# Kernel optimization log

Measured on AMD Instinct MI355X. Metric: run time of the kernel, lower is better.

Reference implementation:

```python
import jax, jax.numpy as jnp
import numpy as np

H, W = 64, 64

def _fft_mask(h, w):
    # matches torch: W -> W//2+1 for rfft; linspace(-1,1,H) x linspace(0,1,W//2+1)
    wr = w // 2 + 1
    ys = np.linspace(-1.0, 1.0, h)
    xs = np.linspace(0.0, 1.0, wr)
    Y, X = np.meshgrid(ys, xs, indexing='ij')
    return (np.abs(X) < 0.1) | (np.abs(Y) < 0.1) | (X ** 2 + Y ** 2 <= 0.4 ** 2)

_MASK = _fft_mask(H, W)
_IY, _IX = np.nonzero(_MASK)            # static gather indices, K = mask.sum()
_K = int(_MASK.sum())


def setup_inputs() -> dict:
    key = jax.random.key(0)
    k1, k2, k3 = jax.random.split(key, 3)
    S, P, C = 16, 256, 3
    enc_dim = 1024
    mask_dim = 6 * _K                    # real+imag, C=3 channels -> 2*3*K
    x = jax.random.normal(k1, (S, P, C, H, W), dtype=jnp.float32)
    bc_mask = jnp.zeros((H, W), dtype=bool)
    proj_w = jax.random.normal(k2, (enc_dim, mask_dim), dtype=jnp.float32) / np.sqrt(mask_dim)
    proj_b = jax.random.normal(k3, (enc_dim,), dtype=jnp.float32) * 0.01
    return {"x": x, "bc_mask": bc_mask, "proj_w": proj_w, "proj_b": proj_b}


def reference(x, bc_mask, proj_w, proj_b):
    S, P, C = x.shape[0], x.shape[1], x.shape[2]
    fft_x = jnp.fft.rfft2(x)                       # (S,P,C,H,W//2+1) complex
    fft_x = jnp.fft.fftshift(fft_x, axes=-2)       # shift along H
    # boolean-mask gather (row-major over (H, W//2+1) per (s,p,c)), then flatten C*K
    filt = fft_x[..., _IY, _IX]                    # (S,P,C,K)
    filt = filt.reshape(S, P, C * _K)
    feats = jnp.concatenate([jnp.real(filt), jnp.imag(filt)], axis=-1)  # (S,P,6K)
    return feats @ proj_w.T + proj_b               # (S,P,enc_dim)
```

## Files before the change

### kernel.cpp

```cpp
#include <hip/hip_runtime.h>
#include <hip/hip_bf16.h>
#include <math.h>

typedef float f32x4 __attribute__((ext_vector_type(4)));
typedef __bf16 bf16x8 __attribute__((ext_vector_type(8)));

#define PI2 6.283185307179586

static __device__ __forceinline__ unsigned short f2b(float f) {
  __hip_bfloat16 h = __float2bfloat16(f);
  return reinterpret_cast<unsigned short&>(h);
}

__global__ __launch_bounds__(256) void setup_tables_kernel(
    unsigned short* __restrict__ post16, __hip_bfloat16* __restrict__ Tt,
    __hip_bfloat16* __restrict__ Ub) {
  const int tid = threadIdx.x;
  __shared__ int cnt[64];
  __shared__ int pref[64];

  if (tid < 64) {
    int i = tid;
    double ys = -1.0 + (double)i * (2.0 / 63.0);
    int cRow = 0;
    for (int j = 0; j < 33; ++j) {
      double xs = (double)j / 32.0;
      bool m = (fabs(xs) < 0.1) || (fabs(ys) < 0.1) || (xs * xs + ys * ys <= 0.16);
      cRow += m ? 1 : 0;
    }
    cnt[i] = cRow;
  }
  __syncthreads();
  if (tid == 0) {
    int s = 0;
    for (int i = 0; i < 64; ++i) { pref[i] = s; s += cnt[i]; }
  }
  __syncthreads();
  if (tid < 64) {
    int i = tid;
    int k = pref[i];
    double ys = -1.0 + (double)i * (2.0 / 63.0);
    for (int j = 0; j < 36; ++j) {
      unsigned short v = 0xFFFFu;
      if (j < 33) {
        double xs = (double)j / 32.0;
        bool m = (fabs(xs) < 0.1) || (fabs(ys) < 0.1) || (xs * xs + ys * ys <= 0.16);
        if (m) v = (unsigned short)(k++);
      }
      post16[i * 36 + j] = v;
    }
  }

  for (int idx = tid; idx < 80 * 64; idx += 256) {
    int n = idx >> 6, w = idx & 63;
    float v = 0.0f;
    if (n < 33) {
      int r = (n * w) & 63;
      v = cosf((float)(PI2 / 64.0) * (float)r);
    } else if (n >= 40 && n < 73) {
      int r = ((n - 40) * w) & 63;
      v = -sinf((float)(PI2 / 64.0) * (float)r);
    }
    Tt[idx] = __float2bfloat16(v);
  }

  for (int idx = tid; idx < 128 * 128; idx += 256) {
    int up = idx >> 7, kk = idx & 127;
    int u = up & 63;
    int vfreq = (u + 32) & 63;
    int h = kk & 63;
    int r = (vfreq * h) & 63;
    float cv, sv;
    __sincosf((float)(PI2 / 64.0) * (float)r, &sv, &cv);
    float val;
    if (up < 64) val = (kk < 64) ? cv : sv;
    else         val = (kk < 64) ? -sv : cv;
    int off = up * 256 + (((kk >> 3) ^ (up & 15)) * 16) + (kk & 7) * 2;
    *reinterpret_cast<unsigned short*>((char*)Ub + off) = f2b(val);
  }
}

__global__ __launch_bounds__(256) void wconv_kernel(
    const float* __restrict__ W, __hip_bfloat16* __restrict__ wB,
    int N, int Kd, int Kp) {
  int total = N * Kp;
  for (int idx = blockIdx.x * 256 + threadIdx.x; idx < total; idx += gridDim.x * 256) {
    int e = idx / Kp;
    int f = idx - e * Kp;
    float v = (f < Kd) ? W[(size_t)e * Kd + f] : 0.0f;
    wB[idx] = __float2bfloat16(v);
  }
}

__global__ __launch_bounds__(256, 4) void s1_kernel(
    const float* __restrict__ x,
    const __hip_bfloat16* __restrict__ Tt,
    unsigned int* __restrict__ S2) {
  __shared__ __align__(16) char lds[2 * 8704];
  const int tid = threadIdx.x;
  const int lane = tid & 63;
  const int w = tid >> 6;
  const int wi = w >> 1;
  const int wp = w & 1;
  const int l4 = lane & 15;
  const int q = lane >> 4;
  const int img = blockIdx.x * 2 + wi;
  char* ibuf = lds + wi * 8704;

  {
    const float* xi = x + (size_t)img * 4096;
    float4 st[8];
    #pragma unroll
    for (int r = 0; r < 8; ++r) {
      int row = wp * 32 + r * 4 + q;
      st[r] = *reinterpret_cast<const float4*>(xi + row * 64 + l4 * 4);
    }
    #pragma unroll
    for (int r = 0; r < 8; ++r) {
      int row = wp * 32 + r * 4 + q;
      int off = row * 128 + (((l4 >> 1) ^ (row & 7)) * 16 + (l4 & 1) * 8);
      ushort4 b;
      b.x = f2b(st[r].x); b.y = f2b(st[r].y); b.z = f2b(st[r].z); b.w = f2b(st[r].w);
      *reinterpret_cast<ushort4*>(ibuf + off) = b;
    }
  }

  f32x4 acc1[2][5] = {};
  #pragma unroll
  for (int ks = 0; ks < 2; ++ks) {
    bf16x8 a1[2], b1[5];
    #pragma unroll
    for (int am = 0; am < 2; ++am) {
      int h = wp * 32 + am * 16 + l4;
      int kg = ks * 4 + q;
      a1[am] = *reinterpret_cast<const bf16x8*>(ibuf + h * 128 + ((kg ^ (h & 7)) * 16));
    }
    #pragma unroll
    for (int n = 0; n < 5; ++n) {
      int row = n * 16 + l4;
      b1[n] = *reinterpret_cast<const bf16x8*>(
          (const char*)Tt + row * 128 + ks * 64 + q * 16);
    }
    #pragma unroll
    for (int am = 0; am < 2; ++am)
      #pragma unroll
      for (int n = 0; n < 5; ++n)
        acc1[am][n] = __builtin_amdgcn_mfma_f32_16x16x32_bf16(a1[am], b1[n], acc1[am][n], 0, 0, 0);
  }

  __syncthreads();

  #pragma unroll
  for (int n = 0; n < 5; ++n) {
    int col = n * 16 + l4;
    bool isRe = (col < 33);
    bool isIm = (col >= 40 && col < 73);
    if (!(isRe || isIm)) continue;
    int j = isRe ? col : (col - 40);
    #pragma unroll
    for (int am = 0; am < 2; ++am) {
      int h0 = wp * 32 + am * 16 + q * 4;
      int kk0 = isRe ? h0 : (h0 + 64);
      int off = j * 256 + (((kk0 >> 3) ^ (j & 15)) * 16 + (kk0 & 7) * 2);
      ushort4 b;
      b.x = f2b(acc1[am][n][0]); b.y = f2b(acc1[am][n][1]);
      b.z = f2b(acc1[am][n][2]); b.w = f2b(acc1[am][n][3]);
      *reinterpret_cast<ushort4*>(ibuf + off) = b;
    }
  }

  __syncthreads();

  {
    const int t2 = tid & 127;
    unsigned int* dst = S2 + (size_t)img * 2112;
    const char* src = ibuf;
    #pragma unroll
    for (int ii = 0; ii < 17; ++ii) {
      int i = ii * 128 + t2;
      if (i < 2112) {
        int j = i >> 6, dw = i & 63;
        unsigned int v = *reinterpret_cast<const unsigned int*>(
            src + j * 256 + (((dw >> 2) ^ (j & 15)) * 16) + (dw & 3) * 4);
        dst[j * 64 + dw] = v;
      }
    }
  }
}

__global__ __launch_bounds__(256, 3) void s2_kernel(
    const char* __restrict__ S2,
    const __hip_bfloat16* __restrict__ Ub,
    const unsigned short* __restrict__ post16,
    __hip_bfloat16* __restrict__ feats,
    int K, int Kp) {
  __shared__ __align__(16) char lds[32768 + 4608 + 4 * 2176];
  const int tid = threadIdx.x;
  const int lane = tid & 63;
  const int w = tid >> 6;
  const int l4 = lane & 15;
  const int q = lane >> 4;
  char* ubl = lds;
  unsigned short* postl = (unsigned short*)(lds + 32768);
  unsigned short* fbs = (unsigned short*)(lds + 32768 + 4608 + w * 2176);

  {
    #pragma unroll
    for (int i = 0; i < 8; ++i) {
      const char* g = (const char*)Ub + (size_t)(i * 256 + w * 64 + lane) * 16;
      char* l = ubl + (size_t)(i * 256 + w * 64) * 16;
      __builtin_amdgcn_global_load_lds(
          (const __attribute__((address_space(1))) void*)g,
          (__attribute__((address_space(3))) void*)l, 16, 0, 0);
    }
    const unsigned int* src = reinterpret_cast<const unsigned int*>(post16);
    unsigned int* dst = reinterpret_cast<unsigned int*>(postl);
    #pragma unroll
    for (int i = 0; i < 5; ++i) {
      int idx = i * 256 + tid;
      if (idx < 1152) dst[idx] = src[idx];
    }
  }
  asm volatile("s_waitcnt vmcnt(0)" ::: "memory");
  __syncthreads();

  const int img = blockIdx.x * 4 + w;
  const int sp = img / 3;
  const int c = img - sp * 3;
  const char* Bimg = S2 + (size_t)img * 8448;

  f32x4 acc[8][3] = {};
  #pragma unroll
  for (int ks = 0; ks < 4; ++ks) {
    bf16x8 bfr[3];
    #pragma unroll
    for (int n = 0; n < 3; ++n) {
      bfr[n] = *reinterpret_cast<const bf16x8*>(
          Bimg + (n * 16 + l4) * 256 + ks * 64 + q * 16);
    }
    #pragma unroll
    for (int m = 0; m < 8; ++m) {
      int row = m * 16 + l4;
      bf16x8 afr = *reinterpret_cast<const bf16x8*>(
          ubl + row * 256 + (((ks * 4 + q) ^ (row & 15)) * 16));
      #pragma unroll
      for (int n = 0; n < 3; ++n)
        acc[m][n] = __builtin_amdgcn_mfma_f32_16x16x32_bf16(afr, bfr[n], acc[m][n], 0, 0, 0);
    }
  }

  #pragma unroll
  for (int n = 0; n < 3; ++n) {
    int col = n * 16 + l4;
    if (col > 32) continue;
    #pragma unroll
    for (int m = 0; m < 8; ++m) {
      #pragma unroll
      for (int r = 0; r < 4; ++r) {
        int row = m * 16 + q * 4 + r;
        int u = row & 63;
        int base = (row >> 6) ? K : 0;
        unsigned short k = postl[u * 36 + col];
        if (k != 0xFFFFu)
          fbs[base + k] = f2b(acc[m][n][r]);
      }
    }
  }

  {
    size_t obase = (size_t)sp * Kp;
    const unsigned int* fb = reinterpret_cast<const unsigned int*>(fbs);
    unsigned int* gRe = reinterpret_cast<unsigned int*>(feats + obase + (size_t)c * K);
    unsigned int* gIm = reinterpret_cast<unsigned int*>(feats + obase + (size_t)3 * K + (size_t)c * K);
    const int KD2 = K / 2;
    for (int i = lane; i < KD2; i += 64) {
      gRe[i] = fb[i];
      gIm[i] = fb[KD2 + i];
    }
    if (c == 2) {
      unsigned int* gp = reinterpret_cast<unsigned int*>(feats + obase + (size_t)6 * K);
      int padDw = (Kp - 6 * K) / 2;
      if (lane < padDw) gp[lane] = 0u;
    }
  }
}

#define BM 128
#define BN 128
#define BKK 64

__global__ __launch_bounds__(256) void gemm_bias_kernel(
    const __hip_bfloat16* __restrict__ A, const __hip_bfloat16* __restrict__ B,
    const float* __restrict__ bias, float* __restrict__ C,
    int M, int N, int Kp) {
  __shared__ __align__(16) unsigned short As[BM * BKK];
  __shared__ __align__(16) unsigned short Bs[BN * BKK];

  const int tid = threadIdx.x;
  const int lane = tid & 63;
  const int wid = tid >> 6;
  const int wm = wid & 1;
  const int wn = wid >> 1;
  const int nbm = M / BM;
  const int bm = blockIdx.x % nbm;
  const int bn = blockIdx.x / nbm;
  const int row0A = bm * BM;
  const int row0B = bn * BN;

  f32x4 acc[4][4] = {};

  for (int k0 = 0; k0 < Kp; k0 += BKK) {
    #pragma unroll
    for (int i = 0; i < 4; ++i) {
      int qc = i * 256 + tid;
      int r = qc >> 3;
      int cb = (qc & 7) * 16;
      const char* gA = (const char*)A + ((size_t)(row0A + r) * Kp + k0) * 2 + cb;
      const char* gB = (const char*)B + ((size_t)(row0B + r) * Kp + k0) * 2 + cb;
      char* lA = (char*)As + (size_t)(i * 256 + wid * 64) * 16;
      char* lB = (char*)Bs + (size_t)(i * 256 + wid * 64) * 16;
      __builtin_amdgcn_global_load_lds((const __attribute__((address_space(1))) void*)gA,
                                       (__attribute__((address_space(3))) void*)lA, 16, 0, 0);
      __builtin_amdgcn_global_load_lds((const __attribute__((address_space(1))) void*)gB,
                                       (__attribute__((address_space(3))) void*)lB, 16, 0, 0);
    }
    __syncthreads();

    #pragma unroll
    for (int kk = 0; kk < 2; ++kk) {
      bf16x8 afr[4], bfr[4];
      const int ke = kk * 32 + (lane >> 4) * 8;
      #pragma unroll
      for (int m = 0; m < 4; ++m) {
        int rowA = wm * 64 + m * 16 + (lane & 15);
        afr[m] = *reinterpret_cast<const bf16x8*>(&As[rowA * BKK + ke]);
      }
      #pragma unroll
      for (int n = 0; n < 4; ++n) {
        int rowB = wn * 64 + n * 16 + (lane & 15);
        bfr[n] = *reinterpret_cast<const bf16x8*>(&Bs[rowB * BKK + ke]);
      }
      #pragma unroll
      for (int m = 0; m < 4; ++m)
        #pragma unroll
        for (int n = 0; n < 4; ++n)
          acc[m][n] = __builtin_amdgcn_mfma_f32_16x16x32_bf16(afr[m], bfr[n], acc[m][n], 0, 0, 0);
    }
    __syncthreads();
  }

  #pragma unroll
  for (int n = 0; n < 4; ++n) {
    int gcol = row0B + wn * 64 + n * 16 + (lane & 15);
    float bv = bias[gcol];
    #pragma unroll
    for (int m = 0; m < 4; ++m) {
      int grow0 = row0A + wm * 64 + m * 16 + (lane >> 4) * 4;
      #pragma unroll
      for (int r = 0; r < 4; ++r) {
        C[(size_t)(grow0 + r) * N + gcol] = acc[m][n][r] + bv;
      }
    }
  }
}

extern "C" void kernel_launch(void* const* d_in, const int* in_sizes, int n_in,
                              void* d_out, int out_size, void* d_ws, size_t ws_size,
                              hipStream_t stream) {
  const float* x = (const float*)d_in[0];
  const float* W = (const float*)d_in[2];
  const float* bias = (const float*)d_in[3];
  float* out = (float*)d_out;

  const int ENC = in_sizes[3];
  const int Kd = in_sizes[2] / ENC;
  const int K = Kd / 6;
  const int NIMG = in_sizes[0] / 4096;
  const int SP = NIMG / 3;
  const int Kp = (Kd + 63) & ~63;

  char* ws = (char*)d_ws;
  unsigned short* post16 = (unsigned short*)ws;
  __hip_bfloat16* Tt = (__hip_bfloat16*)(ws + 9216);
  __hip_bfloat16* Ub = (__hip_bfloat16*)(ws + 19456);
  __hip_bfloat16* wB = (__hip_bfloat16*)(ws + 52224);
  size_t wBytes = (size_t)ENC * Kp * 2;
  __hip_bfloat16* feats = (__hip_bfloat16*)(ws + 52224 + wBytes);
  size_t featsBytes = (size_t)SP * Kp * 2;
  char* S2 = ws + 52224 + wBytes + featsBytes;

  setup_tables_kernel<<<1, 256, 0, stream>>>(post16, Tt, Ub);
  wconv_kernel<<<1024, 256, 0, stream>>>(W, wB, ENC, Kd, Kp);
  s1_kernel<<<NIMG / 2, 256, 0, stream>>>(x, Tt, (unsigned int*)S2);
  s2_kernel<<<NIMG / 4, 256, 0, stream>>>(S2, Ub, post16, feats, K, Kp);
  gemm_bias_kernel<<<(SP / BM) * (ENC / BN), 256, 0, stream>>>(feats, wB, bias, out, SP, ENC, Kp);
}
```

Measured before the change: 204.8 us.

## Stage per-image S2 tile into LDS via async loads, keep swizzled layout in global

The producer kernel now writes its swizzled LDS buffer straight to global memory instead of un-swizzling it. The s2 kernel copies each wave's whole image tile (8448 bytes) into LDS with global_load_lds next to the Ub table load, then reads B fragments from LDS using the XOR swizzle. This replaces scattered 16-byte global loads with coalesced async copies and bank-conflict-free LDS reads. The extra LDS per block lowers the occupancy hint from 3 to 2 blocks per CU.

```diff
diff --git a/kernel.cpp b/kernel.cpp
--- a/kernel.cpp
+++ b/kernel.cpp
@@ -174,27 +174,24 @@
   {
     const int t2 = tid & 127;
     unsigned int* dst = S2 + (size_t)img * 2112;
-    const char* src = ibuf;
+    const unsigned int* src = reinterpret_cast<const unsigned int*>(ibuf);
     #pragma unroll
     for (int ii = 0; ii < 17; ++ii) {
       int i = ii * 128 + t2;
-      if (i < 2112) {
-        int j = i >> 6, dw = i & 63;
-        unsigned int v = *reinterpret_cast<const unsigned int*>(
-            src + j * 256 + (((dw >> 2) ^ (j & 15)) * 16) + (dw & 3) * 4);
-        dst[j * 64 + dw] = v;
-      }
-    }
-  }
-}
-
-__global__ __launch_bounds__(256, 3) void s2_kernel(
+      if (i < 2112) dst[i] = src[i];
+    }
+  }
+}
+
+#define S2B 8448
+
+__global__ __launch_bounds__(256, 2) void s2_kernel(
     const char* __restrict__ S2,
     const __hip_bfloat16* __restrict__ Ub,
     const unsigned short* __restrict__ post16,
     __hip_bfloat16* __restrict__ feats,
     int K, int Kp) {
-  __shared__ __align__(16) char lds[32768 + 4608 + 4 * 2176];
+  __shared__ __align__(16) char lds[32768 + 4608 + 4 * S2B + 4 * 2176];
   const int tid = threadIdx.x;
   const int lane = tid & 63;
   const int w = tid >> 6;
@@ -202,17 +199,38 @@
   const int q = lane >> 4;
   char* ubl = lds;
   unsigned short* postl = (unsigned short*)(lds + 32768);
-  unsigned short* fbs = (unsigned short*)(lds + 32768 + 4608 + w * 2176);
-
+  char* s2l = lds + 32768 + 4608 + w * S2B;
+  unsigned short* fbs = (unsigned short*)(lds + 32768 + 4608 + 4 * S2B + w * 2176);
+
+  const int img = blockIdx.x * 4 + w;
+  const int sp = img / 3;
+  const int c = img - sp * 3;
+  const char* simg = S2 + (size_t)img * S2B;
+
+  #pragma unroll
+  for (int i = 0; i < 8; ++i) {
+    const char* g = (const char*)Ub + (size_t)(w * 8 + i) * 1024 + lane * 16;
+    char* l = ubl + (size_t)(w * 8 + i) * 1024;
+    __builtin_amdgcn_global_load_lds(
+        (const __attribute__((address_space(1))) void*)g,
+        (__attribute__((address_space(3))) void*)l, 16, 0, 0);
+  }
+  #pragma unroll
+  for (int i = 0; i < 8; ++i) {
+    const char* g = simg + i * 1024 + lane * 16;
+    char* l = s2l + i * 1024;
+    __builtin_amdgcn_global_load_lds(
+        (const __attribute__((address_space(1))) void*)g,
+        (__attribute__((address_space(3))) void*)l, 16, 0, 0);
+  }
   {
-    #pragma unroll
-    for (int i = 0; i < 8; ++i) {
-      const char* g = (const char*)Ub + (size_t)(i * 256 + w * 64 + lane) * 16;
-      char* l = ubl + (size_t)(i * 256 + w * 64) * 16;
-      __builtin_amdgcn_global_load_lds(
-          (const __attribute__((address_space(1))) void*)g,
-          (__attribute__((address_space(3))) void*)l, 16, 0, 0);
-    }
+    const char* g = simg + 8192 + lane * 4;
+    char* l = s2l + 8192;
+    __builtin_amdgcn_global_load_lds(
+        (const __attribute__((address_space(1))) void*)g,
+        (__attribute__((address_space(3))) void*)l, 4, 0, 0);
+  }
+  {
     const unsigned int* src = reinterpret_cast<const unsigned int*>(post16);
     unsigned int* dst = reinterpret_cast<unsigned int*>(postl);
     #pragma unroll
@@ -224,25 +242,21 @@
   asm volatile("s_waitcnt vmcnt(0)" ::: "memory");
   __syncthreads();
 
-  const int img = blockIdx.x * 4 + w;
-  const int sp = img / 3;
-  const int c = img - sp * 3;
-  const char* Bimg = S2 + (size_t)img * 8448;
-
   f32x4 acc[8][3] = {};
   #pragma unroll
   for (int ks = 0; ks < 4; ++ks) {
+    const int kg = ks * 4 + q;
     bf16x8 bfr[3];
     #pragma unroll
     for (int n = 0; n < 3; ++n) {
-      bfr[n] = *reinterpret_cast<const bf16x8*>(
-          Bimg + (n * 16 + l4) * 256 + ks * 64 + q * 16);
+      int j = n * 16 + l4;
+      bfr[n] = *reinterpret_cast<const bf16x8*>(s2l + j * 256 + ((kg ^ (j & 15)) * 16));
     }
     #pragma unroll
     for (int m = 0; m < 8; ++m) {
       int row = m * 16 + l4;
       bf16x8 afr = *reinterpret_cast<const bf16x8*>(
-          ubl + row * 256 + (((ks * 4 + q) ^ (row & 15)) * 16));
+          ubl + row * 256 + ((kg ^ (row & 15)) * 16));
       #pragma unroll
       for (int n = 0; n < 3; ++n)
         acc[m][n] = __builtin_amdgcn_mfma_f32_16x16x32_bf16(afr, bfr[n], acc[m][n], 0, 0, 0);
```

New measurement: 210.4 us. 1.03x slower.
